# Kernel tuning notes

Hardware: AMD Instinct MI355X
Metric: run time of the kernel (lower is better)

## Reference

```python
import jax, jax.numpy as jnp
import numpy as np

NEG_SLOPE = 0.01  # torch F.leaky_relu default negative_slope


def setup_inputs() -> dict:
    key = jax.random.key(0)
    ks = jax.random.split(key, 8)
    n_nodes, n_edges, in_f, out_f = 50000, 600000, 128, 128
    src_h = jax.random.normal(ks[0], (n_nodes, in_f), dtype=jnp.float32)
    self_h = jax.random.normal(ks[1], (n_nodes, out_f), dtype=jnp.float32)
    src_idx = jax.random.randint(ks[2], (n_edges,), 0, n_nodes, dtype=jnp.int64 if jax.config.jax_enable_x64 else jnp.int32)
    dst_idx = jax.random.randint(ks[3], (n_edges,), 0, n_nodes, dtype=jnp.int64 if jax.config.jax_enable_x64 else jnp.int32)
    W = jax.random.normal(ks[4], (in_f, out_f), dtype=jnp.float32) / np.sqrt(in_f)
    b = jax.random.normal(ks[5], (out_f,), dtype=jnp.float32) * 0.01
    attn_W = jax.random.normal(ks[6], (2 * out_f, 1), dtype=jnp.float32) / np.sqrt(2 * out_f)
    attn_b = jax.random.normal(ks[7], (1,), dtype=jnp.float32) * 0.01
    return {"src_h": src_h, "self_h": self_h, "src_idx": src_idx, "dst_idx": dst_idx,
            "W": W, "b": b, "attn_W": attn_W, "attn_b": attn_b}


def reference(src_h, self_h, src_idx, dst_idx, W, b, attn_W, attn_b):
    # Per-edge gather of source node features, then linear: z1 = Linear(src['h'])
    z1 = src_h[src_idx] @ W + b                      # [E, out_f]
    # Concat with gathered destination self_h, then attention linear + leaky_relu.
    # Split the concat-matmul to avoid materializing the [E, 2*out_f] concat twice:
    # a = [z1 | self_h[dst]] @ attn_W + attn_b
    Wa_z, Wa_s = attn_W[: z1.shape[1]], attn_W[z1.shape[1]:]
    a = z1 @ Wa_z + self_h[dst_idx] @ Wa_s + attn_b  # [E, 1]
    e = jnp.where(a >= 0, a, NEG_SLOPE * a)          # leaky_relu
    return z1, e
```

## Files before the change

### kernel.cpp

```cpp
#include <hip/hip_runtime.h>
#include <hip/hip_bf16.h>

#define F 128
#define TM 32
#define NEG_SLOPE 0.01f

typedef float vfloat4 __attribute__((ext_vector_type(4)));

__global__ __launch_bounds__(256) void node_kernel(
    const float* __restrict__ src_h,
    const float* __restrict__ self_h,
    const float* __restrict__ W,
    const float* __restrict__ b,
    const float* __restrict__ attn_W,
    float* __restrict__ Y,
    float* __restrict__ yz,
    float* __restrict__ ss,
    int N)
{
    __shared__ float Wl[F * F];
    __shared__ float Al[TM * F];

    const int t = threadIdx.x;
    const int row0 = blockIdx.x * TM;

    for (int i = t * 4; i < F * F; i += 256 * 4) {
        *(float4*)&Wl[i] = *(const float4*)&W[i];
    }
    for (int i = t; i < TM * F / 4; i += 256) {
        const int r  = i >> 5;
        const int c4 = i & 31;
        const int gr = row0 + r;
        float4 v = make_float4(0.f, 0.f, 0.f, 0.f);
        if (gr < N) v = *(const float4*)&src_h[(size_t)gr * F + c4 * 4];
        *(float4*)&Al[r * F + c4 * 4] = v;
    }
    __syncthreads();

    const int colgrp = t & 31;
    const int rowgrp = t >> 5;
    const int c0 = colgrp * 4;
    const int r0 = rowgrp * 4;

    float acc[4][4] = {};

    #pragma unroll 4
    for (int k = 0; k < F; k += 4) {
        const float4 w0 = *(const float4*)&Wl[(k + 0) * F + c0];
        const float4 w1 = *(const float4*)&Wl[(k + 1) * F + c0];
        const float4 w2 = *(const float4*)&Wl[(k + 2) * F + c0];
        const float4 w3 = *(const float4*)&Wl[(k + 3) * F + c0];
        #pragma unroll
        for (int i = 0; i < 4; i++) {
            const float4 a = *(const float4*)&Al[(r0 + i) * F + k];
            acc[i][0] += a.x * w0.x + a.y * w1.x + a.z * w2.x + a.w * w3.x;
            acc[i][1] += a.x * w0.y + a.y * w1.y + a.z * w2.y + a.w * w3.y;
            acc[i][2] += a.x * w0.z + a.y * w1.z + a.z * w2.z + a.w * w3.z;
            acc[i][3] += a.x * w0.w + a.y * w1.w + a.z * w2.w + a.w * w3.w;
        }
    }

    const float4 bb  = *(const float4*)&b[c0];
    const float4 waz = *(const float4*)&attn_W[c0];
    const float4 was = *(const float4*)&attn_W[F + c0];

    #pragma unroll
    for (int i = 0; i < 4; i++) {
        const int gr = row0 + r0 + i;
        float4 o;
        o.x = acc[i][0] + bb.x;
        o.y = acc[i][1] + bb.y;
        o.z = acc[i][2] + bb.z;
        o.w = acc[i][3] + bb.w;

        float pz = o.x * waz.x + o.y * waz.y + o.z * waz.z + o.w * waz.w;

        float ps = 0.f;
        if (gr < N) {
            const float4 s = *(const float4*)&self_h[(size_t)gr * F + c0];
            ps = s.x * was.x + s.y * was.y + s.z * was.z + s.w * was.w;
        }

        #pragma unroll
        for (int m = 16; m >= 1; m >>= 1) {
            pz += __shfl_xor(pz, m, 32);
            ps += __shfl_xor(ps, m, 32);
        }

        if (gr < N) {
            *(float4*)&Y[(size_t)gr * F + c0] = o;
            if (colgrp == 0) {
                yz[gr] = pz;
                ss[gr] = ps;
            }
        }
    }
}

#define EDGE_BLOCKS 2048

__global__ __launch_bounds__(256) void edge_kernel(
    const int* __restrict__ src_idx,
    const int* __restrict__ dst_idx,
    const float* __restrict__ Y,
    const float* __restrict__ yz,
    const float* __restrict__ ss,
    const float* __restrict__ attn_b,
    float* __restrict__ z1,
    float* __restrict__ e_out,
    int E)
{
    const int lane = threadIdx.x & 31;
    const int g    = blockIdx.x * 8 + (threadIdx.x >> 5);
    const int nG   = EDGE_BLOCKS * 8;
    const float ab = attn_b[0];

    for (int e = g; e < E; e += nG) {
        const int s = src_idx[e];
        const vfloat4 v = *(const vfloat4*)&Y[(size_t)s * F + lane * 4];
        __builtin_nontemporal_store(v, (vfloat4*)&z1[(size_t)e * F + lane * 4]);

        if (lane == 0) {
            const int d = dst_idx[e];
            const float a = yz[s] + ss[d] + ab;
            __builtin_nontemporal_store((a >= 0.f) ? a : NEG_SLOPE * a,
                                        &e_out[e]);
        }
    }
}

extern "C" void kernel_launch(void* const* d_in, const int* in_sizes, int n_in,
                              void* d_out, int out_size, void* d_ws, size_t ws_size,
                              hipStream_t stream)
{
    const float* src_h  = (const float*)d_in[0];
    const float* self_h = (const float*)d_in[1];
    const int*   src_idx = (const int*)d_in[2];
    const int*   dst_idx = (const int*)d_in[3];
    const float* W      = (const float*)d_in[4];
    const float* b      = (const float*)d_in[5];
    const float* attn_W = (const float*)d_in[6];
    const float* attn_b = (const float*)d_in[7];

    const int N = in_sizes[0] / F;
    const int E = in_sizes[2];

    float* z1    = (float*)d_out;
    float* e_out = (float*)d_out + (size_t)E * F;

    float* Y  = (float*)d_ws;
    float* yz = Y + (size_t)N * F;
    float* ss = yz + N;

    node_kernel<<<dim3((N + TM - 1) / TM), 256, 0, stream>>>(
        src_h, self_h, W, b, attn_W, Y, yz, ss, N);

    edge_kernel<<<dim3(EDGE_BLOCKS), 256, 0, stream>>>(
        src_idx, dst_idx, Y, yz, ss, attn_b, z1, e_out, E);
}
```

Measured before the change: 470.9 us.

## Stream W in K-chunks with register prefetch to shrink node-kernel LDS

The node kernel no longer stages all of W (64KB) in shared memory. It holds a 32-row chunk and prefetches the next chunk into registers while the current one is multiplied, with syncs between chunks. This cuts LDS per block from 80KB to 32KB so more blocks can be resident per CU, and launch bounds now request 4 blocks per CU. The cost is extra barriers and repeated W loads from global/L2 per block. The e_out store is also switched from nontemporal to a normal store.

```diff
diff --git a/kernel.cpp b/kernel.cpp
--- a/kernel.cpp
+++ b/kernel.cpp
@@ -3,11 +3,12 @@
 
 #define F 128
 #define TM 32
+#define KC 32
 #define NEG_SLOPE 0.01f
 
 typedef float vfloat4 __attribute__((ext_vector_type(4)));
 
-__global__ __launch_bounds__(256) void node_kernel(
+__global__ __launch_bounds__(256, 4) void node_kernel(
     const float* __restrict__ src_h,
     const float* __restrict__ self_h,
     const float* __restrict__ W,
@@ -18,15 +19,12 @@
     float* __restrict__ ss,
     int N)
 {
-    __shared__ float Wl[F * F];
+    __shared__ float Wl[KC * F];
     __shared__ float Al[TM * F];
 
     const int t = threadIdx.x;
     const int row0 = blockIdx.x * TM;
 
-    for (int i = t * 4; i < F * F; i += 256 * 4) {
-        *(float4*)&Wl[i] = *(const float4*)&W[i];
-    }
     for (int i = t; i < TM * F / 4; i += 256) {
         const int r  = i >> 5;
         const int c4 = i & 31;
@@ -35,6 +33,14 @@
         if (gr < N) v = *(const float4*)&src_h[(size_t)gr * F + c4 * 4];
         *(float4*)&Al[r * F + c4 * 4] = v;
     }
+
+    float4 wpre[4];
+    #pragma unroll
+    for (int j = 0; j < 4; j++)
+        wpre[j] = *(const float4*)&W[(size_t)(t + j * 256) * 4];
+    #pragma unroll
+    for (int j = 0; j < 4; j++)
+        *(float4*)&Wl[(t + j * 256) * 4] = wpre[j];
     __syncthreads();
 
     const int colgrp = t & 31;
@@ -44,19 +50,37 @@
 
     float acc[4][4] = {};
 
-    #pragma unroll 4
-    for (int k = 0; k < F; k += 4) {
-        const float4 w0 = *(const float4*)&Wl[(k + 0) * F + c0];
-        const float4 w1 = *(const float4*)&Wl[(k + 1) * F + c0];
-        const float4 w2 = *(const float4*)&Wl[(k + 2) * F + c0];
-        const float4 w3 = *(const float4*)&Wl[(k + 3) * F + c0];
-        #pragma unroll
-        for (int i = 0; i < 4; i++) {
-            const float4 a = *(const float4*)&Al[(r0 + i) * F + k];
-            acc[i][0] += a.x * w0.x + a.y * w1.x + a.z * w2.x + a.w * w3.x;
-            acc[i][1] += a.x * w0.y + a.y * w1.y + a.z * w2.y + a.w * w3.y;
-            acc[i][2] += a.x * w0.z + a.y * w1.z + a.z * w2.z + a.w * w3.z;
-            acc[i][3] += a.x * w0.w + a.y * w1.w + a.z * w2.w + a.w * w3.w;
+    for (int c = 0; c < F / KC; ++c) {
+        if (c + 1 < F / KC) {
+            const float* Wn = &W[(size_t)(c + 1) * KC * F];
+            #pragma unroll
+            for (int j = 0; j < 4; j++)
+                wpre[j] = *(const float4*)&Wn[(t + j * 256) * 4];
+        }
+
+        const int kbase = c * KC;
+        #pragma unroll 4
+        for (int k = 0; k < KC; k += 4) {
+            const float4 w0 = *(const float4*)&Wl[(k + 0) * F + c0];
+            const float4 w1 = *(const float4*)&Wl[(k + 1) * F + c0];
+            const float4 w2 = *(const float4*)&Wl[(k + 2) * F + c0];
+            const float4 w3 = *(const float4*)&Wl[(k + 3) * F + c0];
+            #pragma unroll
+            for (int i = 0; i < 4; i++) {
+                const float4 a = *(const float4*)&Al[(r0 + i) * F + kbase + k];
+                acc[i][0] += a.x * w0.x + a.y * w1.x + a.z * w2.x + a.w * w3.x;
+                acc[i][1] += a.x * w0.y + a.y * w1.y + a.z * w2.y + a.w * w3.y;
+                acc[i][2] += a.x * w0.z + a.y * w1.z + a.z * w2.z + a.w * w3.z;
+                acc[i][3] += a.x * w0.w + a.y * w1.w + a.z * w2.w + a.w * w3.w;
+            }
+        }
+
+        __syncthreads();
+        if (c + 1 < F / KC) {
+            #pragma unroll
+            for (int j = 0; j < 4; j++)
+                *(float4*)&Wl[(t + j * 256) * 4] = wpre[j];
+            __syncthreads();
         }
     }
 
@@ -123,8 +147,7 @@
         if (lane == 0) {
             const int d = dst_idx[e];
             const float a = yz[s] + ss[d] + ab;
-            __builtin_nontemporal_store((a >= 0.f) ? a : NEG_SLOPE * a,
-                                        &e_out[e]);
+            e_out[e] = (a >= 0.f) ? a : NEG_SLOPE * a;
         }
     }
 }
```

Result: no change. 474.8 us (+0.8%).

## Stream W in K-chunks via direct global-to-LDS loads in node kernel

Applied to the files above, without the earlier changes.

Shrinks the node kernel's shared W buffer from the full 128x128 matrix to 32-row chunks. W chunks, and full src_h tiles, are loaded with the global_load_lds builtin, which writes straight into LDS instead of going through registers. The smaller LDS footprint is meant to allow more blocks per CU. The cost is extra block-wide barriers per chunk with no double buffering, so those loads are exposed. The edge kernel, likely the dominant cost, is unchanged.

```diff
diff --git a/kernel.cpp b/kernel.cpp
--- a/kernel.cpp
+++ b/kernel.cpp
@@ -3,6 +3,7 @@
 
 #define F 128
 #define TM 32
+#define KC 32
 #define NEG_SLOPE 0.01f
 
 typedef float vfloat4 __attribute__((ext_vector_type(4)));
@@ -18,22 +19,43 @@
     float* __restrict__ ss,
     int N)
 {
-    __shared__ float Wl[F * F];
+    __shared__ float Wl[KC * F];
     __shared__ float Al[TM * F];
 
-    const int t = threadIdx.x;
+    const int t    = threadIdx.x;
+    const int lane = t & 63;
+    const int w    = t >> 6;
     const int row0 = blockIdx.x * TM;
 
-    for (int i = t * 4; i < F * F; i += 256 * 4) {
-        *(float4*)&Wl[i] = *(const float4*)&W[i];
-    }
-    for (int i = t; i < TM * F / 4; i += 256) {
-        const int r  = i >> 5;
-        const int c4 = i & 31;
-        const int gr = row0 + r;
-        float4 v = make_float4(0.f, 0.f, 0.f, 0.f);
-        if (gr < N) v = *(const float4*)&src_h[(size_t)gr * F + c4 * 4];
-        *(float4*)&Al[r * F + c4 * 4] = v;
+    if (row0 + TM <= N) {
+        #pragma unroll
+        for (int j = 0; j < 4; ++j) {
+            const int m = w * 4 + j;
+            __builtin_amdgcn_global_load_lds(
+                (const __attribute__((address_space(1))) void*)
+                    &src_h[(size_t)row0 * F + m * 256 + lane * 4],
+                (__attribute__((address_space(3))) void*)&Al[m * 256],
+                16, 0, 0);
+        }
+    } else {
+        for (int i = t; i < TM * F / 4; i += 256) {
+            const int r  = i >> 5;
+            const int c4 = i & 31;
+            const int gr = row0 + r;
+            float4 v = make_float4(0.f, 0.f, 0.f, 0.f);
+            if (gr < N) v = *(const float4*)&src_h[(size_t)gr * F + c4 * 4];
+            *(float4*)&Al[r * F + c4 * 4] = v;
+        }
+    }
+
+    #pragma unroll
+    for (int j = 0; j < 4; ++j) {
+        const int m = w * 4 + j;
+        __builtin_amdgcn_global_load_lds(
+            (const __attribute__((address_space(1))) void*)
+                &W[m * 256 + lane * 4],
+            (__attribute__((address_space(3))) void*)&Wl[m * 256],
+            16, 0, 0);
     }
     __syncthreads();
 
@@ -44,20 +66,38 @@
 
     float acc[4][4] = {};
 
-    #pragma unroll 4
-    for (int k = 0; k < F; k += 4) {
-        const float4 w0 = *(const float4*)&Wl[(k + 0) * F + c0];
-        const float4 w1 = *(const float4*)&Wl[(k + 1) * F + c0];
-        const float4 w2 = *(const float4*)&Wl[(k + 2) * F + c0];
-        const float4 w3 = *(const float4*)&Wl[(k + 3) * F + c0];
+    for (int c = 0; ; ++c) {
+        const int kbase = c * KC;
+
+        #pragma unroll 2
+        for (int k = 0; k < KC; k += 4) {
+            const float4 w0 = *(const float4*)&Wl[(k + 0) * F + c0];
+            const float4 w1 = *(const float4*)&Wl[(k + 1) * F + c0];
+            const float4 w2 = *(const float4*)&Wl[(k + 2) * F + c0];
+            const float4 w3 = *(const float4*)&Wl[(k + 3) * F + c0];
+            #pragma unroll
+            for (int i = 0; i < 4; i++) {
+                const float4 a = *(const float4*)&Al[(r0 + i) * F + kbase + k];
+                acc[i][0] += a.x * w0.x + a.y * w1.x + a.z * w2.x + a.w * w3.x;
+                acc[i][1] += a.x * w0.y + a.y * w1.y + a.z * w2.y + a.w * w3.y;
+                acc[i][2] += a.x * w0.z + a.y * w1.z + a.z * w2.z + a.w * w3.z;
+                acc[i][3] += a.x * w0.w + a.y * w1.w + a.z * w2.w + a.w * w3.w;
+            }
+        }
+
+        if (c == F / KC - 1) break;
+
+        __syncthreads();
         #pragma unroll
-        for (int i = 0; i < 4; i++) {
-            const float4 a = *(const float4*)&Al[(r0 + i) * F + k];
-            acc[i][0] += a.x * w0.x + a.y * w1.x + a.z * w2.x + a.w * w3.x;
-            acc[i][1] += a.x * w0.y + a.y * w1.y + a.z * w2.y + a.w * w3.y;
-            acc[i][2] += a.x * w0.z + a.y * w1.z + a.z * w2.z + a.w * w3.z;
-            acc[i][3] += a.x * w0.w + a.y * w1.w + a.z * w2.w + a.w * w3.w;
-        }
+        for (int j = 0; j < 4; ++j) {
+            const int m = w * 4 + j;
+            __builtin_amdgcn_global_load_lds(
+                (const __attribute__((address_space(1))) void*)
+                    &W[(size_t)(c + 1) * KC * F + m * 256 + lane * 4],
+                (__attribute__((address_space(3))) void*)&Wl[m * 256],
+                16, 0, 0);
+        }
+        __syncthreads();
     }
 
     const float4 bb  = *(const float4*)&b[c0];
```

After: 436.4 us. 7.3% less time.
